# Kernel tuning notes

Measured on AMD Instinct MI355X. Metric: run time of the kernel, lower is better.

The kernel has to match this reference:

```python
import jax, jax.numpy as jnp
import numpy as np

N, E, D, HID, OUT, R = 100000, 640000, 128, 128, 128, 8


def setup_inputs() -> dict:
    key = jax.random.key(0)
    ks = jax.random.split(key, 12)
    x = jax.random.normal(ks[0], (N, D), dtype=jnp.float32)
    src = jax.random.randint(ks[1], (E,), 0, N)
    dst = jax.random.randint(ks[2], (E,), 0, N)
    etype = jax.random.randint(ks[3], (E,), 0, R)
    s = 0.05
    W_rel = jax.random.normal(ks[4], (R, D, OUT), dtype=jnp.float32) * s
    loop_w = jax.random.normal(ks[5], (D, OUT), dtype=jnp.float32) * s
    rel_bias = jax.random.normal(ks[6], (OUT,), dtype=jnp.float32) * s
    W1 = jax.random.normal(ks[7], (D + HID, 2 * HID), dtype=jnp.float32) * s
    b1 = jax.random.normal(ks[8], (2 * HID,), dtype=jnp.float32) * s
    W2 = jax.random.normal(ks[9], (D + 2 * HID, OUT), dtype=jnp.float32) * s
    b2 = jax.random.normal(ks[10], (OUT,), dtype=jnp.float32) * s
    return {"x": x, "src": src, "dst": dst, "etype": etype,
            "W_rel": W_rel, "loop_w": loop_w, "rel_bias": rel_bias,
            "W1": W1, "b1": b1, "W2": W2, "b2": b2}


def reference(x, src, dst, etype, W_rel, loop_w, rel_bias, W1, b1, W2, b2):
    n = x.shape[0]
    # RelGraphConv (low_mem): transform all nodes once per relation, then
    # gather the (relation, src)-specific message per edge.  [R, N, OUT]
    h_rel = jnp.einsum('nd,rdo->rno', x, W_rel)
    m = h_rel[etype, src]                                   # [E, OUT]
    agg = jax.ops.segment_sum(m, dst, num_segments=n)       # sum at dst
    msg = agg + x @ loop_w + rel_bias                       # self-loop + bias
    # concat-MLP update (is_block=False -> dst_x = x), activation = tanh
    mid = jnp.tanh(jnp.concatenate([x, msg], axis=1) @ W1 + b1)
    return jnp.concatenate([x, mid], axis=1) @ W2 + b2
```

## Files before the change

kernel.cpp:

```cpp
#include <hip/hip_runtime.h>

#define NN 100000
#define NE 640000
#define RR 8
#define NBIN 800000

typedef unsigned short u16;
typedef u16 u16x4 __attribute__((ext_vector_type(4)));
typedef u16 u16x8 __attribute__((ext_vector_type(8)));
typedef __bf16 bf16x8 __attribute__((ext_vector_type(8)));
typedef float f32x4 __attribute__((ext_vector_type(4)));

#define OFF_XB      0u
#define OFF_WT      25600000u
#define OFF_W1T     25894912u
#define OFF_W2T     26025984u
#define OFF_BUCKET  26124288u
#define OFF_CSROFF  28684288u
#define OFF_CUR     31884292u
#define OFF_PSUM    35084292u

__device__ inline u16 f2bf(float f) {
  unsigned u = __float_as_uint(f);
  u += 0x7FFF + ((u >> 16) & 1);
  return (u16)(u >> 16);
}
__device__ inline float bf2f(u16 h) { return __uint_as_float(((unsigned)h) << 16); }

__device__ inline int edge_bin(int d, int r) { return d * 8 + r; }

__global__ void k_cvt_x(const float* __restrict__ x, u16* __restrict__ xb) {
  const int i = (blockIdx.x * 256 + threadIdx.x) * 4;
  const float4 v = *(const float4*)(x + i);
  u16x4 o;
  o.x = f2bf(v.x); o.y = f2bf(v.y); o.z = f2bf(v.z); o.w = f2bf(v.w);
  *(u16x4*)(xb + i) = o;
}

__global__ void k_cvt_wrel(const float* __restrict__ W, const float* __restrict__ Lw,
                           u16* __restrict__ Wt) {
  const int idx = blockIdx.x * 256 + threadIdx.x;
  const int r = idx >> 14, o = (idx >> 7) & 127, d = idx & 127;
  Wt[idx] = f2bf(r < 8 ? W[(r << 14) + (d << 7) + o] : Lw[(d << 7) + o]);
}

__global__ void k_cvt_w1(const float* __restrict__ W1, u16* __restrict__ W1t) {
  const int idx = blockIdx.x * 256 + threadIdx.x;
  const int o = idx >> 8, i = idx & 255;
  W1t[idx] = f2bf(W1[i * 256 + o]);
}

__global__ void k_cvt_w2(const float* __restrict__ W2, u16* __restrict__ W2t) {
  const int idx = blockIdx.x * 256 + threadIdx.x;
  const int o = idx / 384, i = idx % 384;
  W2t[idx] = f2bf(W2[i * 128 + o]);
}

__global__ void k_hist(const int* __restrict__ dst, const int* __restrict__ et,
                       int* __restrict__ cnt) {
  const int e = blockIdx.x * 256 + threadIdx.x;
  if (e < NE) atomicAdd(&cnt[edge_bin(dst[e], et[e])], 1);
}

__global__ void k_scanA(const int* __restrict__ cnt, int* __restrict__ psum) {
  __shared__ int sc[256];
  const int tid = threadIdx.x, base = blockIdx.x * 1024 + tid * 4;
  int s = 0;
#pragma unroll
  for (int t = 0; t < 4; ++t) { const int i = base + t; if (i < NBIN) s += cnt[i]; }
  sc[tid] = s; __syncthreads();
  for (int d = 128; d > 0; d >>= 1) {
    if (tid < d) sc[tid] += sc[tid + d];
    __syncthreads();
  }
  if (tid == 0) psum[blockIdx.x] = sc[0];
}

__global__ void k_scanB(int* __restrict__ psum) {
  __shared__ int sc[1024];
  const int tid = threadIdx.x;
  const int v = (tid < 782) ? psum[tid] : 0;
  sc[tid] = v; __syncthreads();
  for (int d = 1; d < 1024; d <<= 1) {
    const int t = (tid >= d) ? sc[tid - d] : 0;
    __syncthreads();
    sc[tid] += t;
    __syncthreads();
  }
  if (tid < 782) psum[tid] = sc[tid] - v;
}

__global__ void k_scanC(int* __restrict__ cnt , const int* __restrict__ psum,
                        int* __restrict__ off) {
  __shared__ int sc[256];
  const int tid = threadIdx.x, base = blockIdx.x * 1024 + tid * 4;
  int c[4], s = 0;
#pragma unroll
  for (int t = 0; t < 4; ++t) {
    const int i = base + t;
    c[t] = (i < NBIN) ? cnt[i] : 0;
    s += c[t];
  }
  sc[tid] = s; __syncthreads();
  for (int d = 1; d < 256; d <<= 1) {
    const int t = (tid >= d) ? sc[tid - d] : 0;
    __syncthreads();
    sc[tid] += t;
    __syncthreads();
  }
  int run = psum[blockIdx.x] + sc[tid] - s;
#pragma unroll
  for (int t = 0; t < 4; ++t) {
    const int i = base + t;
    if (i < NBIN) { off[i] = run; cnt[i] = run; run += c[t]; }
  }
  if (blockIdx.x == 0 && tid == 0) off[NBIN] = NE;
}

__global__ void k_scatter(const int* __restrict__ src, const int* __restrict__ dst,
                          const int* __restrict__ et, int* __restrict__ cur,
                          unsigned* __restrict__ bucket) {
  const int e = blockIdx.x * 256 + threadIdx.x;
  if (e < NE) {
    const int d = dst[e], r = et[e];
    const int pos = atomicAdd(&cur[edge_bin(d, r)], 1);
    bucket[pos] = (unsigned)src[e] | ((unsigned)r << 17);
  }
}

#define ATS 136
#define WCAP 448
#define NPRE 8
__global__ __launch_bounds__(256, 4) void k_fused(
    const u16* __restrict__ xb, const u16* __restrict__ Wt,
    const int* __restrict__ csroff, const unsigned* __restrict__ bucket,
    const float* __restrict__ rel_bias,
    const u16* __restrict__ W1t, const float* __restrict__ b1,
    const u16* __restrict__ W2t, const float* __restrict__ b2,
    float* __restrict__ out) {
  __shared__ u16 At[4 * 32 * ATS];
  __shared__ unsigned wlds[WCAP];
  const int tid = threadIdx.x;
  const int v0 = blockIdx.x * 32;
  const int wave = tid >> 6, lane = tid & 63;
  const int l16 = lane & 15, quad = lane >> 4;
  const int rt = wave & 1, cb = (wave >> 1) << 6;
  const int grp = tid >> 4, l16g = tid & 15;

  const int gbase = csroff[v0 * 8];
  const int ntot  = csroff[v0 * 8 + 256] - gbase;

  f32x4 acc[4] = {};

  {
    const u16* xp = xb + ((size_t)(v0 + rt * 16 + l16) << 7) + quad * 8;
    bf16x8 afr[4];
#pragma unroll
    for (int t = 0; t < 4; ++t) afr[t] = *(const bf16x8*)(xp + t * 32);
    const u16* wb = Wt + (8 << 14);
#pragma unroll
    for (int c = 0; c < 4; ++c) {
      const u16* wp = wb + (size_t)(cb + c * 16 + l16) * 128 + quad * 8;
#pragma unroll
      for (int t = 0; t < 4; ++t)
        acc[c] = __builtin_amdgcn_mfma_f32_16x16x32_bf16(afr[t], *(const bf16x8*)(wp + t * 32), acc[c], 0, 0, 0);
    }
  }

  {
    const int nst = ntot < WCAP ? ntot : WCAP;
    for (int i = tid; i < nst; i += 256) wlds[i] = bucket[gbase + i];
  }
  __syncthreads();

#pragma unroll
  for (int ph = 0; ph < 2; ++ph) {
    {
      const u16x8 z = {0, 0, 0, 0, 0, 0, 0, 0};
#pragma unroll
      for (int q = 0; q < 4; ++q) {
        *(u16x8*)&At[q * (32 * ATS) + grp * ATS + l16g * 8] = z;
        *(u16x8*)&At[q * (32 * ATS) + (grp + 16) * ATS + l16g * 8] = z;
      }
    }

#pragma unroll
    for (int half = 0; half < 2; ++half) {
      const int node = half * 16 + grp;
      const int pbeg = csroff[v0 * 8 + node * 8 + ph * 4] - gbase;
      const int pend = csroff[v0 * 8 + node * 8 + ph * 4 + 4] - gbase;
      const int n = pend - pbeg;

      unsigned wv[NPRE];
#pragma unroll
      for (int j = 0; j < NPRE; ++j) {
        int p = pbeg + j;
        if (p >= pend) p = pbeg;
        wv[j] = (p < WCAP) ? wlds[p] : bucket[gbase + p];
      }
      u16x8 h[NPRE];
#pragma unroll
      for (int j = 0; j < NPRE; ++j) {
        unsigned row = wv[j] & 0x1FFFFu;
        row = row < NN ? row : 0u;
        h[j] = *(const u16x8*)(xb + ((size_t)row << 7) + l16g * 8);
      }
      float a[8] = {};
      int crel = -1;
#pragma unroll
      for (int j = 0; j < NPRE; ++j) {
        if (j < n) {
          const int r = (int)((wv[j] >> 17) & 7u);
          if (r != crel) {
            if (crel >= 0) {
              u16x8 o;
#pragma unroll
              for (int t = 0; t < 8; ++t) o[t] = f2bf(a[t]);
              *(u16x8*)&At[(crel & 3) * (32 * ATS) + node * ATS + l16g * 8] = o;
            }
#pragma unroll
            for (int t = 0; t < 8; ++t) a[t] = 0.f;
            crel = r;
          }
#pragma unroll
          for (int t = 0; t < 8; ++t) a[t] += bf2f(h[j][t]);
        }
      }
      for (int i = NPRE; i < n; ++i) {
        const int p = pbeg + i;
        const unsigned w = (p < WCAP) ? wlds[p] : bucket[gbase + p];
        const u16x8 hh = *(const u16x8*)(xb + ((size_t)(w & 0x1FFFFu) << 7) + l16g * 8);
        const int r = (int)((w >> 17) & 7u);
        if (r != crel) {
          if (crel >= 0) {
            u16x8 o;
#pragma unroll
            for (int t = 0; t < 8; ++t) o[t] = f2bf(a[t]);
            *(u16x8*)&At[(crel & 3) * (32 * ATS) + node * ATS + l16g * 8] = o;
          }
#pragma unroll
          for (int t = 0; t < 8; ++t) a[t] = 0.f;
          crel = r;
        }
#pragma unroll
        for (int t = 0; t < 8; ++t) a[t] += bf2f(hh[t]);
      }
      if (crel >= 0) {
        u16x8 o;
#pragma unroll
        for (int t = 0; t < 8; ++t) o[t] = f2bf(a[t]);
        *(u16x8*)&At[(crel & 3) * (32 * ATS) + node * ATS + l16g * 8] = o;
      }
    }
    __syncthreads();

#pragma unroll
    for (int q = 0; q < 4; ++q) {
      bf16x8 afr[4];
#pragma unroll
      for (int t = 0; t < 4; ++t)
        afr[t] = *(const bf16x8*)&At[q * (32 * ATS) + (rt * 16 + l16) * ATS + quad * 8 + t * 32];
      const u16* wb = Wt + ((ph * 4 + q) << 14);
#pragma unroll
      for (int c = 0; c < 4; ++c) {
        const u16* wp = wb + (size_t)(cb + c * 16 + l16) * 128 + quad * 8;
#pragma unroll
        for (int t = 0; t < 4; ++t)
          acc[c] = __builtin_amdgcn_mfma_f32_16x16x32_bf16(afr[t], *(const bf16x8*)(wp + t * 32), acc[c], 0, 0, 0);
      }
    }
    __syncthreads();
  }

  u16* Mt = At;
  u16* Ht = At + 32 * 136;
#pragma unroll
  for (int c = 0; c < 4; ++c) {
    const int col = cb + c * 16 + l16;
    const float bias = rel_bias[col];
#pragma unroll
    for (int reg = 0; reg < 4; ++reg) {
      const int row = rt * 16 + quad * 4 + reg;
      Mt[row * 136 + col] = f2bf(acc[c][reg] + bias);
    }
  }
  __syncthreads();

  {
    const int ch = (wave >> 1) << 7;
    f32x4 acc2[8] = {};
#pragma unroll
    for (int kt = 0; kt < 8; ++kt) {
      bf16x8 af;
      if (kt < 4)
        af = *(const bf16x8*)(xb + ((size_t)(v0 + rt * 16 + l16) << 7) + kt * 32 + quad * 8);
      else
        af = *(const bf16x8*)&Mt[(rt * 16 + l16) * 136 + (kt - 4) * 32 + quad * 8];
#pragma unroll
      for (int ct = 0; ct < 8; ++ct) {
        const u16* wp = W1t + (size_t)(ch + ct * 16 + l16) * 256 + kt * 32 + quad * 8;
        acc2[ct] = __builtin_amdgcn_mfma_f32_16x16x32_bf16(af, *(const bf16x8*)(wp), acc2[ct], 0, 0, 0);
      }
    }
#pragma unroll
    for (int ct = 0; ct < 8; ++ct) {
      const int col = ch + ct * 16 + l16;
      const float bias = b1[col];
#pragma unroll
      for (int reg = 0; reg < 4; ++reg) {
        const int row = rt * 16 + quad * 4 + reg;
        Ht[row * 264 + col] = f2bf(tanhf(acc2[ct][reg] + bias));
      }
    }
  }
  __syncthreads();

  {
    f32x4 acc3[4] = {};
#pragma unroll
    for (int kt = 0; kt < 12; ++kt) {
      bf16x8 af;
      if (kt < 4)
        af = *(const bf16x8*)(xb + ((size_t)(v0 + rt * 16 + l16) << 7) + kt * 32 + quad * 8);
      else
        af = *(const bf16x8*)&Ht[(rt * 16 + l16) * 264 + (kt - 4) * 32 + quad * 8];
#pragma unroll
      for (int ct = 0; ct < 4; ++ct) {
        const u16* wp = W2t + (size_t)(cb + ct * 16 + l16) * 384 + kt * 32 + quad * 8;
        acc3[ct] = __builtin_amdgcn_mfma_f32_16x16x32_bf16(af, *(const bf16x8*)(wp), acc3[ct], 0, 0, 0);
      }
    }
#pragma unroll
    for (int ct = 0; ct < 4; ++ct) {
      const int col = cb + ct * 16 + l16;
      const float bias = b2[col];
#pragma unroll
      for (int reg = 0; reg < 4; ++reg) {
        const int row = v0 + rt * 16 + quad * 4 + reg;
        out[(size_t)row * 128 + col] = acc3[ct][reg] + bias;
      }
    }
  }
}

extern "C" void kernel_launch(void* const* d_in, const int* in_sizes, int n_in,
                              void* d_out, int out_size, void* d_ws, size_t ws_size,
                              hipStream_t stream) {
  (void)in_sizes; (void)n_in; (void)out_size; (void)ws_size;
  const float* x        = (const float*)d_in[0];
  const int*   src      = (const int*)d_in[1];
  const int*   dst      = (const int*)d_in[2];
  const int*   et       = (const int*)d_in[3];
  const float* W_rel    = (const float*)d_in[4];
  const float* loop_w   = (const float*)d_in[5];
  const float* rel_bias = (const float*)d_in[6];
  const float* W1       = (const float*)d_in[7];
  const float* b1       = (const float*)d_in[8];
  const float* W2       = (const float*)d_in[9];
  const float* b2       = (const float*)d_in[10];
  float* out = (float*)d_out;

  char* ws = (char*)d_ws;
  u16*      xb     = (u16*)(ws + OFF_XB);
  u16*      Wt     = (u16*)(ws + OFF_WT);
  u16*      W1t    = (u16*)(ws + OFF_W1T);
  u16*      W2t    = (u16*)(ws + OFF_W2T);
  unsigned* bucket = (unsigned*)(ws + OFF_BUCKET);
  int*      csroff = (int*)(ws + OFF_CSROFF);
  int*      cur    = (int*)(ws + OFF_CUR);
  int*      psum   = (int*)(ws + OFF_PSUM);

  hipMemsetAsync(cur, 0, (size_t)NBIN * 4, stream);

  k_cvt_x   <<<(NN * 128) / 1024, 256, 0, stream>>>(x, xb);
  k_cvt_wrel<<<(9 * 16384) / 256, 256, 0, stream>>>(W_rel, loop_w, Wt);
  k_cvt_w1  <<<(256 * 256) / 256, 256, 0, stream>>>(W1, W1t);
  k_cvt_w2  <<<(128 * 384) / 256, 256, 0, stream>>>(W2, W2t);

  k_hist    <<<(NE + 255) / 256, 256, 0, stream>>>(dst, et, cur);
  k_scanA   <<<782, 256, 0, stream>>>(cur, psum);
  k_scanB   <<<1, 1024, 0, stream>>>(psum);
  k_scanC   <<<782, 256, 0, stream>>>(cur, psum, csroff);
  k_scatter <<<(NE + 255) / 256, 256, 0, stream>>>(src, dst, et, cur, bucket);

  k_fused   <<<NN / 32, 256, 0, stream>>>(xb, Wt, csroff, bucket, rel_bias,
                                          W1t, b1, W2t, b2, out);
}
```

Baseline: 611.1 us.

## Stage neighbor row gathers through LDS with async global_load_lds batches

Replaces the register-prefetched gather of source rows (8 upfront plus a serial tail loop) with batches of 4 asynchronous global-to-LDS loads per wave, waited on with vmcnt(0) and then read back from a staging buffer. CSR offsets per half-relation group are also cached in shared memory instead of being reloaded from global memory. The aim is to keep several gathers in flight for every neighbor, not only the first eight, and to cut register pressure. In exchange it adds LDS use, lowers the occupancy hint from 4 to 3, and drains the queue fully for each batch.

Result: slower. 636.0 us (+4.1%).

```diff
diff --git a/kernel.cpp b/kernel.cpp
--- a/kernel.cpp
+++ b/kernel.cpp
@@ -27,6 +27,13 @@
 }
 __device__ inline float bf2f(u16 h) { return __uint_as_float(((unsigned)h) << 16); }
 
+__device__ __forceinline__ void async_row16(const void* g, void* l) {
+  __builtin_amdgcn_global_load_lds(
+      (const __attribute__((address_space(1))) void*)g,
+      (__attribute__((address_space(3))) void*)(unsigned)(unsigned long long)l,
+      16, 0, 0);
+}
+
 __device__ inline int edge_bin(int d, int r) { return d * 8 + r; }
 
 __global__ void k_cvt_x(const float* __restrict__ x, u16* __restrict__ xb) {
@@ -130,8 +137,8 @@
 
 #define ATS 136
 #define WCAP 448
-#define NPRE 8
-__global__ __launch_bounds__(256, 4) void k_fused(
+#define SDEP 4
+__global__ __launch_bounds__(256, 3) void k_fused(
     const u16* __restrict__ xb, const u16* __restrict__ Wt,
     const int* __restrict__ csroff, const unsigned* __restrict__ bucket,
     const float* __restrict__ rel_bias,
@@ -140,12 +147,15 @@
     float* __restrict__ out) {
   __shared__ u16 At[4 * 32 * ATS];
   __shared__ unsigned wlds[WCAP];
+  __shared__ u16 stage[4 * SDEP * 512];
+  __shared__ int coff4[66];
   const int tid = threadIdx.x;
   const int v0 = blockIdx.x * 32;
   const int wave = tid >> 6, lane = tid & 63;
   const int l16 = lane & 15, quad = lane >> 4;
   const int rt = wave & 1, cb = (wave >> 1) << 6;
   const int grp = tid >> 4, l16g = tid & 15;
+  const int gw = grp & 3;
 
   const int gbase = csroff[v0 * 8];
   const int ntot  = csroff[v0 * 8 + 256] - gbase;
@@ -170,6 +180,7 @@
   {
     const int nst = ntot < WCAP ? ntot : WCAP;
     for (int i = tid; i < nst; i += 256) wlds[i] = bucket[gbase + i];
+    if (tid < 65) coff4[tid] = csroff[v0 * 8 + tid * 4];
   }
   __syncthreads();
 
@@ -187,68 +198,58 @@
 #pragma unroll
     for (int half = 0; half < 2; ++half) {
       const int node = half * 16 + grp;
-      const int pbeg = csroff[v0 * 8 + node * 8 + ph * 4] - gbase;
-      const int pend = csroff[v0 * 8 + node * 8 + ph * 4 + 4] - gbase;
+      const int pbeg = coff4[2 * node + ph] - gbase;
+      const int pend = coff4[2 * node + ph + 1] - gbase;
       const int n = pend - pbeg;
 
-      unsigned wv[NPRE];
-#pragma unroll
-      for (int j = 0; j < NPRE; ++j) {
-        int p = pbeg + j;
-        if (p >= pend) p = pbeg;
-        wv[j] = (p < WCAP) ? wlds[p] : bucket[gbase + p];
-      }
-      u16x8 h[NPRE];
-#pragma unroll
-      for (int j = 0; j < NPRE; ++j) {
-        unsigned row = wv[j] & 0x1FFFFu;
-        row = row < NN ? row : 0u;
-        h[j] = *(const u16x8*)(xb + ((size_t)row << 7) + l16g * 8);
-      }
       float a[8] = {};
       int crel = -1;
-#pragma unroll
-      for (int j = 0; j < NPRE; ++j) {
-        if (j < n) {
-          const int r = (int)((wv[j] >> 17) & 7u);
-          if (r != crel) {
-            if (crel >= 0) {
-              u16x8 o;
-#pragma unroll
-              for (int t = 0; t < 8; ++t) o[t] = f2bf(a[t]);
-              *(u16x8*)&At[(crel & 3) * (32 * ATS) + node * ATS + l16g * 8] = o;
+
+      for (int jb = 0; __any(n > jb); jb += SDEP) {
+        unsigned wv[SDEP];
+#pragma unroll
+        for (int t = 0; t < SDEP; ++t) {
+          int p = pbeg + jb + t;
+          p = (p < pend) ? p : pbeg;
+          wv[t] = (p < WCAP) ? wlds[p] : bucket[gbase + p];
+        }
+#pragma unroll
+        for (int t = 0; t < SDEP; ++t) {
+          if (__any(n > jb + t)) {
+            unsigned row = wv[t] & 0x1FFFFu;
+            row = row < NN ? row : 0u;
+            async_row16(xb + ((size_t)row << 7) + l16g * 8,
+                        &stage[(wave * SDEP + t) * 512]);
+          }
+        }
+        asm volatile("s_waitcnt vmcnt(0)" ::: "memory");
+#pragma unroll
+        for (int t = 0; t < SDEP; ++t) {
+          const int j = jb + t;
+          if (j < n) {
+            const int r = (int)((wv[t] >> 17) & 7u);
+            if (r != crel) {
+              if (crel >= 0) {
+                u16x8 o;
+#pragma unroll
+                for (int u = 0; u < 8; ++u) o[u] = f2bf(a[u]);
+                *(u16x8*)&At[(crel & 3) * (32 * ATS) + node * ATS + l16g * 8] = o;
+              }
+#pragma unroll
+              for (int u = 0; u < 8; ++u) a[u] = 0.f;
+              crel = r;
             }
-#pragma unroll
-            for (int t = 0; t < 8; ++t) a[t] = 0.f;
-            crel = r;
+            const u16x8 hh = *(const u16x8*)&stage[(wave * SDEP + t) * 512 + gw * 128 + l16g * 8];
+#pragma unroll
+            for (int u = 0; u < 8; ++u) a[u] += bf2f(hh[u]);
           }
-#pragma unroll
-          for (int t = 0; t < 8; ++t) a[t] += bf2f(h[j][t]);
         }
-      }
-      for (int i = NPRE; i < n; ++i) {
-        const int p = pbeg + i;
-        const unsigned w = (p < WCAP) ? wlds[p] : bucket[gbase + p];
-        const u16x8 hh = *(const u16x8*)(xb + ((size_t)(w & 0x1FFFFu) << 7) + l16g * 8);
-        const int r = (int)((w >> 17) & 7u);
-        if (r != crel) {
-          if (crel >= 0) {
-            u16x8 o;
-#pragma unroll
-            for (int t = 0; t < 8; ++t) o[t] = f2bf(a[t]);
-            *(u16x8*)&At[(crel & 3) * (32 * ATS) + node * ATS + l16g * 8] = o;
-          }
-#pragma unroll
-          for (int t = 0; t < 8; ++t) a[t] = 0.f;
-          crel = r;
-        }
-#pragma unroll
-        for (int t = 0; t < 8; ++t) a[t] += bf2f(hh[t]);
+        asm volatile("s_waitcnt lgkmcnt(0)" ::: "memory");
       }
       if (crel >= 0) {
         u16x8 o;
 #pragma unroll
-        for (int t = 0; t < 8; ++t) o[t] = f2bf(a[t]);
+        for (int u = 0; u < 8; ++u) o[u] = f2bf(a[u]);
         *(u16x8*)&At[(crel & 3) * (32 * ATS) + node * ATS + l16g * 8] = o;
       }
     }
```
